# Kernel optimization log

Measured on AMD Instinct MI355X. Metric: run time of the kernel, lower is better.

The kernel has to match this reference:

```python
import jax, jax.numpy as jnp
import numpy as np

B, C, H, W = 4, 64, 256, 256
P, PRIOR, HID, HEADS, NPROMPT = 4, 64, 128, 4, 4
TOKEN = C * P * P  # 1024
RATIO = 0.25


def _patchify(x):
    b, c, h, w = x.shape
    gh, gw = h // P, w // P
    t = x.reshape(b, c, gh, P, gw, P).transpose(0, 2, 4, 1, 3, 5).reshape(b, gh * gw, c * P * P)
    return t, (b, c, gh, gw)


def _unpatchify(t, meta):
    b, c, gh, gw = meta
    return t.reshape(b, gh, gw, c, P, P).transpose(0, 3, 1, 4, 2, 5).reshape(b, c, gh * P, gw * P)


def _coords(gh, gw):
    ys = (jnp.arange(gh, dtype=jnp.float32) + 0.5) / gh
    xs = (jnp.arange(gw, dtype=jnp.float32) + 0.5) / gw
    yy, xx = jnp.meshgrid(ys, xs, indexing='ij')
    return jnp.stack([yy.ravel(), xx.ravel()], axis=-1)  # [N, 2]


def setup_inputs():
    key = jax.random.key(0)
    ks = iter(jax.random.split(key, 32))
    rn = lambda *s: jax.random.normal(next(ks), s, jnp.float32)
    w = lambda *s: rn(*s) * 0.02
    z = lambda *s: jnp.zeros(s, jnp.float32)
    return dict(
        vis_feat=rn(B, C, H, W),
        ir_feat=rn(B, C, H, W),
        prompt_bank=w(NPROMPT, PRIOR),
        Wr=w(2 * C, NPROMPT), br=z(NPROMPT),
        br_Wtok=w(2, 2 * TOKEN, HID), br_Wpri=w(2, PRIOR, HID), br_Wco=w(2, 2, HID),
        br_bs=z(2, HID), br_Wout=w(2, HID), br_bout=z(2),
        br_Wq=w(2, TOKEN, HID), br_Wk=w(2, TOKEN, HID), br_Wv=w(2, TOKEN, HID),
        br_Wo=w(2, HID, TOKEN), br_Wint=w(2, PRIOR, HID),
        br_Wbyp=w(2, 2 * TOKEN, TOKEN), br_bbyp=z(2, TOKEN),
        conv1_w=w(C, C, 3, 3), conv1_b=z(C),
        conv2_w=w(C, C, 3, 3), conv2_b=z(C),
        Wa1=w(PRIOR, 2 * C), ba1=z(2 * C),
        Wa2=w(2 * C, 2 * C), ba2=z(2 * C),
    )


def reference(vis_feat, ir_feat, prompt_bank, Wr, br, br_Wtok, br_Wpri, br_Wco, br_bs, br_Wout, br_bout, br_Wq, br_Wk, br_Wv, br_Wo, br_Wint, br_Wbyp, br_bbyp, conv1_w, conv1_b, conv2_w, conv2_b, Wa1, ba1, Wa2, ba2):
    # intent router: pooled features -> prompt mixture -> intent vector
    pooled = jnp.concatenate([vis_feat.mean((2, 3)), ir_feat.mean((2, 3))], -1)  # [B, 2C]
    prompt_weight = jax.nn.softmax(pooled @ Wr + br, -1)  # [B, NPROMPT]
    intent = prompt_weight @ prompt_bank  # [B, PRIOR]

    def split(x):
        F = jnp.fft.fft2(x)
        return jnp.abs(F), jnp.angle(F)

    vamp, vph = split(vis_feat)
    iamp, iph = split(ir_feat)

    def fuse(vm, im, i):
        vt, meta = _patchify(vm)
        it_, _ = _patchify(im)
        b, c, gh, gw = meta
        n = gh * gw
        coords = _coords(gh, gw)
        # token score net: tokens + intent + coord embedding -> scalar score per token
        h = (jnp.concatenate([vt, it_], -1) @ br_Wtok[i]
             + (intent @ br_Wpri[i])[:, None, :]
             + (coords @ br_Wco[i])[None] + br_bs[i])
        score = jax.nn.gelu(h) @ br_Wout[i] + br_bout[i]  # [B, N]
        k = max(1, int(n * RATIO))
        topk_val, topk_idx = jax.lax.top_k(score, k)
        gth = lambda t: jnp.take_along_axis(t, topk_idx[:, :, None], axis=1)
        vs, irs = gth(vt), gth(it_)  # [B, k, TOKEN]
        # selected-token cross attention (vis queries, ir keys/values), intent-modulated
        dh = HID // HEADS
        hd = lambda x, Wm: (x @ Wm).reshape(b, k, HEADS, dh)
        q, kk, vv = hd(vs, br_Wq[i]), hd(irs, br_Wk[i]), hd(irs, br_Wv[i])
        attn = jax.nn.softmax(jnp.einsum('bqhd,bkhd->bhqk', q, kk) / jnp.float32(np.sqrt(dh)), -1)
        o = jnp.einsum('bhqk,bkhd->bqhd', attn, vv).reshape(b, k, HID)
        o = o + (intent @ br_Wint[i])[:, None, :]
        fused_sel = vs + o @ br_Wo[i]  # [B, k, TOKEN]
        # lightweight bypass on all tokens (gated blend), then scatter selected back
        g = jax.nn.sigmoid(jnp.concatenate([vt, it_], -1) @ br_Wbyp[i] + br_bbyp[i])
        full = g * vt + (1.0 - g) * it_
        full = full.at[jnp.arange(b)[:, None], topk_idx].set(fused_sel)
        return _unpatchify(full, meta)

    famp = fuse(vamp, iamp, 0)
    fph = fuse(vph, iph, 1)
    fph = jnp.arctan2(jnp.sin(fph), jnp.cos(fph))  # phase wrap to (-pi, pi]
    spec = jax.lax.complex(famp * jnp.cos(fph), famp * jnp.sin(fph))
    spatial = jnp.fft.ifft2(spec).real

    conv = lambda x, wgt, bia: jax.lax.conv_general_dilated(
        x, wgt, (1, 1), 'SAME', dimension_numbers=('NCHW', 'OIHW', 'NCHW')) + bia[None, :, None, None]
    y = conv(jax.nn.relu(conv(spatial, conv1_w, conv1_b)), conv2_w, conv2_b)
    aff = jax.nn.gelu(intent @ Wa1 + ba1) @ Wa2 + ba2  # [B, 2C]
    gamma, beta = aff[:, :C], aff[:, C:]
    y = y * (1.0 + 0.1 * jnp.tanh(gamma))[:, :, None, None] + 0.1 * beta[:, :, None, None]
    return y + 0.5 * (vis_feat + ir_feat)
```

## Files before the change

kernel.cpp:

```cpp
#include <hip/hip_runtime.h>

typedef unsigned int uint;
typedef unsigned short ushort;
typedef unsigned long long u64;
typedef __attribute__((ext_vector_type(8))) short short8;
typedef __attribute__((ext_vector_type(4))) float f32x4;

__device__ __forceinline__ uint brev8(uint x){ return __brev(x) >> 24; }
__device__ __forceinline__ float geluf(float x){
  return 0.5f*x*(1.f + tanhf(0.7978845608028654f*(x + 0.044715f*x*x*x)));
}
__device__ __forceinline__ ushort f2bf(float f){
  unsigned u = __float_as_uint(f);
  unsigned r = u + 0x7FFFu + ((u >> 16) & 1u);
  return (ushort)(r >> 16);
}
__device__ __forceinline__ float bf2f(ushort u){
  return __uint_as_float((uint)u << 16);
}

__global__ __launch_bounds__(256) void kern_pool(const float* __restrict__ vis,
                                                 const float* __restrict__ irf,
                                                 float* __restrict__ pooled){
  __shared__ float red[256];
  int bc = blockIdx.x;
  int b = bc >> 7, cc = bc & 127;
  const float* src = (cc < 64) ? (vis + (size_t)(b*64+cc)*65536)
                               : (irf + (size_t)(b*64+(cc-64))*65536);
  float s = 0.f;
  for (int i = threadIdx.x; i < 65536; i += 256) s += src[i];
  red[threadIdx.x] = s;
  __syncthreads();
  for (int off = 128; off > 0; off >>= 1){
    if (threadIdx.x < off) red[threadIdx.x] += red[threadIdx.x + off];
    __syncthreads();
  }
  if (threadIdx.x == 0) pooled[bc] = red[0] * (1.f/65536.f);
}

__global__ __launch_bounds__(256) void kern_small(const float* __restrict__ pooled,
    const float* __restrict__ Wr, const float* __restrict__ br,
    const float* __restrict__ bank, const float* __restrict__ Wpri,
    const float* __restrict__ Wint, const float* __restrict__ Wa1,
    const float* __restrict__ ba1, const float* __restrict__ Wa2,
    const float* __restrict__ ba2,
    float* __restrict__ IP, float* __restrict__ IPint,
    float* __restrict__ modg, float* __restrict__ modb){
  __shared__ float logit_s[16];
  __shared__ float pw_s[16];
  __shared__ float intent_s[4][64];
  __shared__ float t1_s[4][128];
  int t = threadIdx.x;
  if (t < 16){
    int b = t >> 2, j = t & 3;
    float s = br[j];
    for (int k = 0; k < 128; ++k) s += pooled[b*128+k]*Wr[k*4+j];
    logit_s[t] = s;
  }
  __syncthreads();
  if (t < 4){
    int b = t;
    float m = logit_s[b*4];
    for (int j = 1; j < 4; ++j) m = fmaxf(m, logit_s[b*4+j]);
    float e[4], sum = 0.f;
    for (int j = 0; j < 4; ++j){ e[j] = expf(logit_s[b*4+j]-m); sum += e[j]; }
    for (int j = 0; j < 4; ++j) pw_s[b*4+j] = e[j]/sum;
  }
  __syncthreads();
  {
    int b = t >> 6, p = t & 63;
    float s = 0.f;
    for (int j = 0; j < 4; ++j) s += pw_s[b*4+j]*bank[j*64+p];
    intent_s[b][p] = s;
  }
  __syncthreads();
  for (int o = t; o < 1024; o += 256){
    int i = o >> 9, rem = o & 511, b = rem >> 7, n = rem & 127;
    float s1 = 0.f, s2 = 0.f;
    for (int p = 0; p < 64; ++p){
      float iv = intent_s[b][p];
      s1 += iv * Wpri[(i*64+p)*128 + n];
      s2 += iv * Wint[(i*64+p)*128 + n];
    }
    IP[o] = s1; IPint[o] = s2;
  }
  for (int o = t; o < 512; o += 256){
    int b = o >> 7, n = o & 127;
    float s = ba1[n];
    for (int p = 0; p < 64; ++p) s += intent_s[b][p]*Wa1[p*128+n];
    t1_s[b][n] = geluf(s);
  }
  __syncthreads();
  for (int o = t; o < 512; o += 256){
    int b = o >> 7, n = o & 127;
    float s = ba2[n];
    for (int p = 0; p < 128; ++p) s += t1_s[b][p]*Wa2[p*128+n];
    if (n < 64) modg[b*64+n] = 1.f + 0.1f*tanhf(s);
    else        modb[b*64+(n-64)] = 0.1f*s;
  }
}

__global__ __launch_bounds__(256) void kern_fft_rows_pack(const float* __restrict__ xv,
    const float* __restrict__ xi, float* __restrict__ sre, float* __restrict__ sim){
  __shared__ float re[2][256], im[2][256];
  __shared__ float twr[128], twi[128];
  int t = threadIdx.x;
  if (t < 128){
    float a = -6.2831853071795864f * (float)t * (1.f/256.f);
    sincosf(a, &twi[t], &twr[t]);
  }
  int r = t >> 7, jj = t & 127;
  size_t row = (size_t)blockIdx.x*2 + r;
  {
    const float* vp = xv + row*256;
    const float* ip = xi + row*256;
    re[r][jj] = vp[jj]; re[r][jj+128] = vp[jj+128];
    im[r][jj] = ip[jj]; im[r][jj+128] = ip[jj+128];
  }
  __syncthreads();
  for (int s = 0; s < 8; ++s){
    int half = 128 >> s;
    int j = jj & (half-1);
    int g = jj >> (7-s);
    int k = (g << (8-s)) + j;
    int m = j << s;
    float wc = twr[m], ws = twi[m];
    float are = re[r][k],      aim = im[r][k];
    float bre = re[r][k+half], bim = im[r][k+half];
    re[r][k] = are + bre; im[r][k] = aim + bim;
    float tr = are - bre, ti = aim - bim;
    re[r][k+half] = tr*wc - ti*ws;
    im[r][k+half] = tr*ws + ti*wc;
    __syncthreads();
  }
  {
    float* orp = sre + row*256; float* oip = sim + row*256;
    int w1 = jj, w2 = jj + 128;
    orp[w1] = re[r][brev8(w1)]; oip[w1] = im[r][brev8(w1)];
    orp[w2] = re[r][brev8(w2)]; oip[w2] = im[r][brev8(w2)];
  }
}

__global__ __launch_bounds__(256) void kern_fft_cols_pack(const float* __restrict__ sre,
    const float* __restrict__ sim, ushort* __restrict__ AV, ushort* __restrict__ PV,
    ushort* __restrict__ AI, ushort* __restrict__ PI){
  __shared__ float reL[256*17];
  __shared__ float imL[256*17];
  __shared__ float twr[128], twi[128];
  int t = threadIdx.x;
  if (t < 128){
    float a = -6.2831853071795864f * (float)t * (1.f/256.f);
    sincosf(a, &twi[t], &twr[t]);
  }
  int img = blockIdx.x >> 4;
  int j = blockIdx.x & 15;
  {
    const float* pr = sre + ((size_t)img*256 + t)*256;
    const float* pi = sim + ((size_t)img*256 + t)*256;
    int base = t*17;
    float4 a0 = *(const float4*)(pr + 8*j);
    float4 a1 = *(const float4*)(pr + 8*j + 4);
    float4 c0 = *(const float4*)(pi + 8*j);
    float4 c1 = *(const float4*)(pi + 8*j + 4);
    reL[base+0]=a0.x; reL[base+1]=a0.y; reL[base+2]=a0.z; reL[base+3]=a0.w;
    reL[base+4]=a1.x; reL[base+5]=a1.y; reL[base+6]=a1.z; reL[base+7]=a1.w;
    imL[base+0]=c0.x; imL[base+1]=c0.y; imL[base+2]=c0.z; imL[base+3]=c0.w;
    imL[base+4]=c1.x; imL[base+5]=c1.y; imL[base+6]=c1.z; imL[base+7]=c1.w;
    if (j == 0){
      reL[base+8] = pr[128]; imL[base+8] = pi[128];
      float4 b0 = *(const float4*)(pr + 248);
      float4 b1 = *(const float4*)(pr + 252);
      float4 d0 = *(const float4*)(pi + 248);
      float4 d1 = *(const float4*)(pi + 252);
      reL[base+9]=b0.y;  reL[base+10]=b0.z; reL[base+11]=b0.w;
      reL[base+12]=b1.x; reL[base+13]=b1.y; reL[base+14]=b1.z; reL[base+15]=b1.w;
      imL[base+9]=d0.y;  imL[base+10]=d0.z; imL[base+11]=d0.w;
      imL[base+12]=d1.x; imL[base+13]=d1.y; imL[base+14]=d1.z; imL[base+15]=d1.w;
    } else {
      float4 b0 = *(const float4*)(pr + 248 - 8*j);
      float4 b1 = *(const float4*)(pr + 252 - 8*j);
      float4 d0 = *(const float4*)(pi + 248 - 8*j);
      float4 d1 = *(const float4*)(pi + 252 - 8*j);
      reL[base+8]=b0.y;  reL[base+9]=b0.z;  reL[base+10]=b0.w;
      reL[base+11]=b1.x; reL[base+12]=b1.y; reL[base+13]=b1.z; reL[base+14]=b1.w;
      reL[base+15]=pr[256 - 8*j];
      imL[base+8]=d0.y;  imL[base+9]=d0.z;  imL[base+10]=d0.w;
      imL[base+11]=d1.x; imL[base+12]=d1.y; imL[base+13]=d1.z; imL[base+14]=d1.w;
      imL[base+15]=pi[256 - 8*j];
    }
  }
  __syncthreads();
  int col = t & 15, tb = t >> 4;
  for (int s = 0; s < 8; ++s){
    int half = 128 >> s;
    #pragma unroll
    for (int it = 0; it < 8; ++it){
      int tj = tb + it*16;
      int jl = tj & (half-1);
      int g = tj >> (7-s);
      int k = (g << (8-s)) + jl;
      int m = jl << s;
      float wc = twr[m], ws = twi[m];
      int i0 = k*17 + col, i1 = (k+half)*17 + col;
      float are = reL[i0], aim = imL[i0];
      float bre = reL[i1], bim = imL[i1];
      reL[i0] = are + bre; imL[i0] = aim + bim;
      float tr = are - bre, ti = aim - bim;
      reL[i1] = tr*wc - ti*ws;
      imL[i1] = tr*ws + ti*wc;
    }
    __syncthreads();
  }
  int b = img >> 6, cimg = img & 63;
  int u = t;
  int su  = (int)brev8((uint)u) * 17;
  int smu = (int)brev8((uint)((256 - u) & 255)) * 17;
  #pragma unroll
  for (int c = 0; c < 16; ++c){
    int v, mc;
    if (j == 0){
      v  = (c < 8) ? c : ((c == 8) ? 128 : 240 + c);
      mc = (c == 0) ? 0 : ((c == 8) ? 8 : 16 - c);
    } else {
      v  = (c < 8) ? (8*j + c) : (241 - 8*j + c);
      mc = 15 - c;
    }
    float re1 = reL[su + c],  im1 = imL[su + c];
    float re2 = reL[smu + mc], im2 = imL[smu + mc];
    float vr = 0.5f*(re1 + re2), vi = 0.5f*(im1 - im2);
    float jr = 0.5f*(im1 + im2), ji = 0.5f*(re2 - re1);
    float aV = sqrtf(vr*vr + vi*vi), pVh = atan2f(vi, vr);
    float aI = sqrtf(jr*jr + ji*ji), pIh = atan2f(ji, jr);
    size_t addr = ((size_t)(b*4096 + (u>>2)*64 + (v>>2)))*1024
                + cimg*16 + (u&3)*4 + (v&3);
    AV[addr] = f2bf(aV); PV[addr] = f2bf(pVh);
    AI[addr] = f2bf(aI); PI[addr] = f2bf(pIh);
  }
}

__global__ __launch_bounds__(256) void kern_ifft_rows_spec(const float* __restrict__ famp,
    const float* __restrict__ fph, float* __restrict__ sre, float* __restrict__ sim){
  __shared__ float re[4][256], im[4][256];
  __shared__ float twr[128], twi[128];
  int t = threadIdx.x;
  if (t < 128){
    float a = -6.2831853071795864f * (float)t * (1.f/256.f);
    sincosf(a, &twi[t], &twr[t]);
  }
  int R = blockIdx.x * 4;
  {
    int r = t >> 6, q = t & 63;
    int row = R + r;
    int bc = row >> 8, h = row & 255;
    int b = bc >> 6, c = bc & 63;
    size_t addr = ((size_t)(b*4096 + (h>>2)*64 + q))*1024 + c*16 + (h&3)*4;
    float4 a4 = *(const float4*)(famp + addr);
    float4 p4 = *(const float4*)(fph + addr);
    float sn, cs;
    sincosf(p4.x, &sn, &cs); re[r][4*q+0] = a4.x*cs; im[r][4*q+0] = a4.x*sn;
    sincosf(p4.y, &sn, &cs); re[r][4*q+1] = a4.y*cs; im[r][4*q+1] = a4.y*sn;
    sincosf(p4.z, &sn, &cs); re[r][4*q+2] = a4.z*cs; im[r][4*q+2] = a4.z*sn;
    sincosf(p4.w, &sn, &cs); re[r][4*q+3] = a4.w*cs; im[r][4*q+3] = a4.w*sn;
  }
  __syncthreads();
  for (int s = 0; s < 8; ++s){
    int half = 128 >> s;
    #pragma unroll
    for (int bi0 = 0; bi0 < 2; ++bi0){
      int bi = t + bi0*256;
      int r = bi >> 7, tj = bi & 127;
      int j = tj & (half-1);
      int g = tj >> (7-s);
      int k = (g << (8-s)) + j;
      int m = j << s;
      float wc = twr[m], ws = -twi[m];
      float are = re[r][k],      aim = im[r][k];
      float bre = re[r][k+half], bim = im[r][k+half];
      re[r][k] = are + bre; im[r][k] = aim + bim;
      float tr = are - bre, ti = aim - bim;
      re[r][k+half] = tr*wc - ti*ws;
      im[r][k+half] = tr*ws + ti*wc;
    }
    __syncthreads();
  }
  {
    int r = t >> 6, q = t & 63;
    size_t row = (size_t)R + r;
    float4 vr, vi;
    vr.x = re[r][brev8(4*q+0)]; vi.x = im[r][brev8(4*q+0)];
    vr.y = re[r][brev8(4*q+1)]; vi.y = im[r][brev8(4*q+1)];
    vr.z = re[r][brev8(4*q+2)]; vi.z = im[r][brev8(4*q+2)];
    vr.w = re[r][brev8(4*q+3)]; vi.w = im[r][brev8(4*q+3)];
    *(float4*)(sre + row*256 + 4*q) = vr;
    *(float4*)(sim + row*256 + 4*q) = vi;
  }
}

__global__ __launch_bounds__(256) void kern_fft_cols_inv(const float* __restrict__ sre,
    const float* __restrict__ sim, float* __restrict__ out0){
  __shared__ float reL[256*17];
  __shared__ float imL[256*17];
  __shared__ float twr[128], twi[128];
  int t = threadIdx.x;
  if (t < 128){
    float a = -6.2831853071795864f * (float)t * (1.f/256.f);
    sincosf(a, &twi[t], &twr[t]);
  }
  int img = blockIdx.x >> 4;
  int c0 = (blockIdx.x & 15) * 16;
  {
    const float* pr = sre + ((size_t)img*256 + t)*256 + c0;
    const float* pi = sim + ((size_t)img*256 + t)*256 + c0;
    #pragma unroll
    for (int p = 0; p < 4; ++p){
      float4 vr = *(const float4*)(pr + 4*p);
      float4 vi = *(const float4*)(pi + 4*p);
      int base = t*17 + 4*p;
      reL[base+0]=vr.x; reL[base+1]=vr.y; reL[base+2]=vr.z; reL[base+3]=vr.w;
      imL[base+0]=vi.x; imL[base+1]=vi.y; imL[base+2]=vi.z; imL[base+3]=vi.w;
    }
  }
  __syncthreads();
  int col = t & 15, tb = t >> 4;
  for (int s = 0; s < 8; ++s){
    int half = 128 >> s;
    #pragma unroll
    for (int it = 0; it < 8; ++it){
      int tj = tb + it*16;
      int j = tj & (half-1);
      int g = tj >> (7-s);
      int k = (g << (8-s)) + j;
      int m = j << s;
      float wc = twr[m];
      float ws = -twi[m];
      int i0 = k*17 + col, i1 = (k+half)*17 + col;
      float are = reL[i0], aim = imL[i0];
      float bre = reL[i1], bim = imL[i1];
      reL[i0] = are + bre; imL[i0] = aim + bim;
      float tr = are - bre, ti = aim - bim;
      reL[i1] = tr*wc - ti*ws;
      imL[i1] = tr*ws + ti*wc;
    }
    __syncthreads();
  }
  int h = t; int src = (int)brev8((uint)h);
  float* op = out0 + ((size_t)img*256 + h)*256 + c0;
  #pragma unroll
  for (int p = 0; p < 4; ++p){
    int base = src*17 + 4*p;
    float4 v;
    v.x = reL[base+0]*(1.f/65536.f);
    v.y = reL[base+1]*(1.f/65536.f);
    v.z = reL[base+2]*(1.f/65536.f);
    v.w = reL[base+3]*(1.f/65536.f);
    *(float4*)(op + 4*p) = v;
  }
}

struct TRS {
  const float* src[10];
  ushort* dst[10];
  int K[10], N[10];
  int start[11];
};
__global__ __launch_bounds__(256) void kern_tr(TRS p){
  __shared__ float lds[32][33];
  int bid = blockIdx.x;
  int e = 0;
  while (bid >= p.start[e+1]) ++e;
  int tloc = bid - p.start[e];
  int tilesN = p.N[e] >> 5;
  int tn = tloc % tilesN, tk = tloc / tilesN;
  int k0 = tk << 5, n0 = tn << 5;
  const float* src = p.src[e];
  ushort* dst = p.dst[e];
  int K = p.K[e], N = p.N[e];
  int r = threadIdx.x >> 5, c = threadIdx.x & 31;
  #pragma unroll
  for (int i = 0; i < 4; ++i)
    lds[r + 8*i][c] = src[(size_t)(k0 + r + 8*i)*N + n0 + c];
  __syncthreads();
  #pragma unroll
  for (int i = 0; i < 4; ++i)
    dst[(size_t)(n0 + r + 8*i)*K + k0 + c] = f2bf(lds[c][r + 8*i]);
}

struct GP2 {
  const ushort* A0[6];
  const ushort* Bt[6];
  float* Cm[6];
  const int* idxp[6];
  int N, K;
};

__global__ __launch_bounds__(256) void kern_mgemm2(GP2 p){
  __shared__ __align__(16) ushort Asb[64*64];
  __shared__ __align__(16) ushort Bsb[128*64];
  __shared__ int idx_s[64];
  int z = blockIdx.z;
  const ushort* A0 = p.A0[z];
  const ushort* Bt = p.Bt[z];
  float* Cm = p.Cm[z];
  int tid = threadIdx.x;
  int m0 = blockIdx.x * 64;
  int n0 = blockIdx.y * 128;
  int lane = tid & 63, w = tid >> 6;
  int wr = w & 1, wc = w >> 1;
  int lr = lane & 15, ql = lane >> 4;

  if (tid < 64){
    int m = m0 + tid;
    idx_s[tid] = p.idxp[z][(m >> 10)*1024 + (m & 1023)];
  }
  __syncthreads();
  int gb = m0 >> 10;

  f32x4 acc[2][4];
  #pragma unroll
  for (int i = 0; i < 2; ++i)
    #pragma unroll
    for (int j = 0; j < 4; ++j) acc[i][j] = (f32x4){0.f,0.f,0.f,0.f};

  int kh = tid & 7;
  int rA = tid >> 3;
  for (int k0 = 0; k0 < p.K; k0 += 64){
    #pragma unroll
    for (int s = 0; s < 2; ++s){
      int m = rA + 32*s;
      const ushort* ap = A0 + ((size_t)(gb << 12) + idx_s[m])*(size_t)p.K + k0 + kh*8;
      short8 v = *(const short8*)ap;
      int byte = m*128 + ((kh*16) ^ ((m & 7)*16));
      *(short8*)((char*)Asb + byte) = v;
    }
    #pragma unroll
    for (int s = 0; s < 4; ++s){
      int n = rA + 32*s;
      short8 v = *(const short8*)(Bt + (size_t)(n0+n)*p.K + k0 + kh*8);
      int byte = n*128 + ((kh*16) ^ ((n & 7)*16));
      *(short8*)((char*)Bsb + byte) = v;
    }
    __syncthreads();
    short8 af[2][2], bf[4][2];
    #pragma unroll
    for (int fm = 0; fm < 2; ++fm){
      int row = wr*32 + fm*16 + lr;
      #pragma unroll
      for (int kq = 0; kq < 2; ++kq){
        int byte = row*128 + ((kq*64 + ql*16) ^ ((row & 7)*16));
        af[fm][kq] = *(const short8*)((const char*)Asb + byte);
      }
    }
    #pragma unroll
    for (int fn = 0; fn < 4; ++fn){
      int row = wc*64 + fn*16 + lr;
      #pragma unroll
      for (int kq = 0; kq < 2; ++kq){
        int byte = row*128 + ((kq*64 + ql*16) ^ ((row & 7)*16));
        bf[fn][kq] = *(const short8*)((const char*)Bsb + byte);
      }
    }
    #pragma unroll
    for (int kq = 0; kq < 2; ++kq)
      #pragma unroll
      for (int fm = 0; fm < 2; ++fm)
        #pragma unroll
        for (int fn = 0; fn < 4; ++fn)
          acc[fm][fn] = __builtin_amdgcn_mfma_f32_16x16x32_bf16(af[fm][kq], bf[fn][kq],
                                                                acc[fm][fn], 0, 0, 0);
    __syncthreads();
  }

  #pragma unroll
  for (int fm = 0; fm < 2; ++fm){
    #pragma unroll
    for (int fn = 0; fn < 4; ++fn){
      int n = n0 + wc*64 + fn*16 + lr;
      #pragma unroll
      for (int reg = 0; reg < 4; ++reg){
        int m = m0 + wr*32 + fm*16 + ql*4 + reg;
        Cm[(size_t)m*p.N + n] = acc[fm][fn][reg];
      }
    }
  }
}

struct HSP {
  const ushort* A0[2];
  const ushort* A1[2];
  const ushort* Bt[2];
  float* score;
  const float* ep0[2];
  const float* ep1[2];
  const float* ep2[2];
  const float* wout;
  const float* bout;
  int Mper;
};

__global__ __launch_bounds__(256) void kern_hscore(HSP p){
  __shared__ __align__(16) ushort Asb[128*64];
  __shared__ __align__(16) ushort Bsb[128*64];
  __shared__ float part[2][128];
  int z = blockIdx.z;
  const ushort* Bt = p.Bt[z];
  int tid = threadIdx.x;
  int m0 = blockIdx.x * 128;
  int lane = tid & 63, w = tid >> 6;
  int wr = w & 1, wc = w >> 1;
  int lr = lane & 15, ql = lane >> 4;

  f32x4 acc[4][4];
  #pragma unroll
  for (int i = 0; i < 4; ++i)
    #pragma unroll
    for (int j = 0; j < 4; ++j) acc[i][j] = (f32x4){0.f,0.f,0.f,0.f};

  int kh = tid & 7;
  int rA = tid >> 3;
  for (int k0 = 0; k0 < 2048; k0 += 64){
    const ushort* Asrc = (k0 < 1024) ? p.A0[z] : p.A1[z];
    int kk = (k0 & 1023) + kh*8;
    #pragma unroll
    for (int s = 0; s < 4; ++s){
      int m = rA + 32*s;
      short8 v = *(const short8*)(Asrc + (size_t)(m0+m)*1024 + kk);
      int byte = m*128 + ((kh*16) ^ ((m & 7)*16));
      *(short8*)((char*)Asb + byte) = v;
    }
    #pragma unroll
    for (int s = 0; s < 4; ++s){
      int n = rA + 32*s;
      short8 v = *(const short8*)(Bt + (size_t)n*2048 + k0 + kh*8);
      int byte = n*128 + ((kh*16) ^ ((n & 7)*16));
      *(short8*)((char*)Bsb + byte) = v;
    }
    __syncthreads();
    short8 af[4][2], bf[4][2];
    #pragma unroll
    for (int fm = 0; fm < 4; ++fm){
      int row = wr*64 + fm*16 + lr;
      #pragma unroll
      for (int kq = 0; kq < 2; ++kq){
        int byte = row*128 + ((kq*64 + ql*16) ^ ((row & 7)*16));
        af[fm][kq] = *(const short8*)((const char*)Asb + byte);
      }
    }
    #pragma unroll
    for (int fn = 0; fn < 4; ++fn){
      int row = wc*64 + fn*16 + lr;
      #pragma unroll
      for (int kq = 0; kq < 2; ++kq){
        int byte = row*128 + ((kq*64 + ql*16) ^ ((row & 7)*16));
        bf[fn][kq] = *(const short8*)((const char*)Bsb + byte);
      }
    }
    #pragma unroll
    for (int kq = 0; kq < 2; ++kq)
      #pragma unroll
      for (int fm = 0; fm < 4; ++fm)
        #pragma unroll
        for (int fn = 0; fn < 4; ++fn)
          acc[fm][fn] = __builtin_amdgcn_mfma_f32_16x16x32_bf16(af[fm][kq], bf[fn][kq],
                                                                acc[fm][fn], 0, 0, 0);
    __syncthreads();
  }

  float wv[4];
  #pragma unroll
  for (int fn = 0; fn < 4; ++fn) wv[fn] = p.wout[z*128 + wc*64 + fn*16 + lr];
  #pragma unroll
  for (int fm = 0; fm < 4; ++fm){
    #pragma unroll
    for (int reg = 0; reg < 4; ++reg){
      int m = m0 + wr*64 + fm*16 + ql*4 + reg;
      int bl = m >> 12, g = m & 4095;
      int gy = g >> 6, gx = g & 63;
      float cy = ((float)gy + 0.5f)*(1.f/64.f);
      float cx = ((float)gx + 0.5f)*(1.f/64.f);
      float ps = 0.f;
      #pragma unroll
      for (int fn = 0; fn < 4; ++fn){
        int n = wc*64 + fn*16 + lr;
        float o = acc[fm][fn][reg] + p.ep0[z][bl*128 + n] + cy*p.ep1[z][n]
                + cx*p.ep1[z][128 + n] + p.ep2[z][n];
        ps += geluf(o)*wv[fn];
      }
      #pragma unroll
      for (int off = 8; off > 0; off >>= 1) ps += __shfl_xor(ps, off);
      if (lr == 0) part[wc][wr*64 + fm*16 + ql*4 + reg] = ps;
    }
  }
  __syncthreads();
  if (tid < 128)
    p.score[(size_t)z*p.Mper + m0 + tid] = part[0][tid] + part[1][tid] + p.bout[z];
}

struct BYP {
  const ushort* A0[2];
  const ushort* A1[2];
  const ushort* Bt[2];
  float* Cm[2];
  const int* nsel[2];
  const float* bias[2];
  const ushort* vt[2];
  const ushort* it[2];
};

__global__ __launch_bounds__(256) void kern_byp(BYP p){
  __shared__ __align__(16) ushort Asb[128*64];
  __shared__ __align__(16) ushort Bsb[128*64];
  __shared__ int idx_s[128];
  int z = blockIdx.z;
  const ushort* Bt = p.Bt[z];
  int tid = threadIdx.x;
  int gb  = blockIdx.x / 24;
  int m0l = (blockIdx.x % 24) * 128;
  int n0 = blockIdx.y * 128;
  int lane = tid & 63, w = tid >> 6;
  int wr = w & 1, wc = w >> 1;
  int lr = lane & 15, ql = lane >> 4;

  if (tid < 128)
    idx_s[tid] = p.nsel[z][(size_t)gb*3072 + m0l + tid];
  __syncthreads();

  f32x4 acc[4][4];
  #pragma unroll
  for (int i = 0; i < 4; ++i)
    #pragma unroll
    for (int j = 0; j < 4; ++j) acc[i][j] = (f32x4){0.f,0.f,0.f,0.f};

  int kh = tid & 7;
  int rA = tid >> 3;
  for (int k0 = 0; k0 < 2048; k0 += 64){
    const ushort* Asrc = (k0 < 1024) ? p.A0[z] : p.A1[z];
    int kk = (k0 & 1023) + kh*8;
    #pragma unroll
    for (int s = 0; s < 4; ++s){
      int m = rA + 32*s;
      size_t grow = (size_t)(gb << 12) + idx_s[m];
      short8 v = *(const short8*)(Asrc + grow*1024 + kk);
      int byte = m*128 + ((kh*16) ^ ((m & 7)*16));
      *(short8*)((char*)Asb + byte) = v;
    }
    #pragma unroll
    for (int s = 0; s < 4; ++s){
      int n = rA + 32*s;
      short8 v = *(const short8*)(Bt + (size_t)(n0+n)*2048 + k0 + kh*8);
      int byte = n*128 + ((kh*16) ^ ((n & 7)*16));
      *(short8*)((char*)Bsb + byte) = v;
    }
    __syncthreads();
    short8 af[4][2], bf[4][2];
    #pragma unroll
    for (int fm = 0; fm < 4; ++fm){
      int row = wr*64 + fm*16 + lr;
      #pragma unroll
      for (int kq = 0; kq < 2; ++kq){
        int byte = row*128 + ((kq*64 + ql*16) ^ ((row & 7)*16));
        af[fm][kq] = *(const short8*)((const char*)Asb + byte);
      }
    }
    #pragma unroll
    for (int fn = 0; fn < 4; ++fn){
      int row = wc*64 + fn*16 + lr;
      #pragma unroll
      for (int kq = 0; kq < 2; ++kq){
        int byte = row*128 + ((kq*64 + ql*16) ^ ((row & 7)*16));
        bf[fn][kq] = *(const short8*)((const char*)Bsb + byte);
      }
    }
    #pragma unroll
    for (int kq = 0; kq < 2; ++kq)
      #pragma unroll
      for (int fm = 0; fm < 4; ++fm)
        #pragma unroll
        for (int fn = 0; fn < 4; ++fn)
          acc[fm][fn] = __builtin_amdgcn_mfma_f32_16x16x32_bf16(af[fm][kq], bf[fn][kq],
                                                                acc[fm][fn], 0, 0, 0);
    __syncthreads();
  }

  float* Cm = p.Cm[z];
  const ushort* vtp = p.vt[z];
  const ushort* itp = p.it[z];
  #pragma unroll
  for (int fm = 0; fm < 4; ++fm){
    #pragma unroll
    for (int fn = 0; fn < 4; ++fn){
      int n = n0 + wc*64 + fn*16 + lr;
      float bia = p.bias[z][n];
      #pragma unroll
      for (int reg = 0; reg < 4; ++reg){
        int mloc = wr*64 + fm*16 + ql*4 + reg;
        size_t off = ((size_t)(gb << 12) + idx_s[mloc])*1024 + n;
        float vt = bf2f(vtp[off]);
        float it = bf2f(itp[off]);
        float gg = 1.f/(1.f + expf(-(acc[fm][fn][reg] + bia)));
        Cm[off] = gg*vt + (1.f-gg)*it;
      }
    }
  }
}

struct SCP {
  const float* A0[2];
  const float* Bm[2];
  float* Cm[2];
  const int* idxp[2];
  const ushort* vtb[2];
};

__global__ __launch_bounds__(256) void kern_scat(SCP p){
  __shared__ __align__(16) ushort Asb[64*40];
  __shared__ __align__(16) ushort Bsb[128*40];
  __shared__ int idx_s[64];
  int z = blockIdx.z;
  const float* A0 = p.A0[z];
  const float* Bm = p.Bm[z];
  float* Cm = p.Cm[z];
  int tid = threadIdx.x;
  int m0 = blockIdx.y * 64;
  int n0 = blockIdx.x * 128;
  int lane = tid & 63, w = tid >> 6;
  int wr = w & 1, wc = w >> 1;
  int lr = lane & 15, ql = lane >> 4;
  if (tid < 64){
    int m = m0 + tid;
    idx_s[tid] = p.idxp[z][(m >> 10)*1024 + (m & 1023)];
  }
  __syncthreads();
  int gb = m0 >> 10;

  f32x4 acc[2][4];
  #pragma unroll
  for (int i = 0; i < 2; ++i)
    #pragma unroll
    for (int j = 0; j < 4; ++j) acc[i][j] = (f32x4){0.f,0.f,0.f,0.f};

  for (int k0 = 0; k0 < 128; k0 += 32){
    {
      int m = tid & 63;
      int khh = (tid >> 6) * 8;
      const float* ap = A0 + (size_t)(m0+m)*128 + k0 + khh;
      float4 f0 = *(const float4*)ap;
      float4 f1 = *(const float4*)(ap + 4);
      short8 v;
      v[0]=(short)f2bf(f0.x); v[1]=(short)f2bf(f0.y);
      v[2]=(short)f2bf(f0.z); v[3]=(short)f2bf(f0.w);
      v[4]=(short)f2bf(f1.x); v[5]=(short)f2bf(f1.y);
      v[6]=(short)f2bf(f1.z); v[7]=(short)f2bf(f1.w);
      *(short8*)&Asb[m*40 + khh] = v;
    }
    #pragma unroll
    for (int e0 = 0; e0 < 512; e0 += 256){
      int e = e0 + tid;
      int n = e & 127;
      int khh = (e >> 7) * 8;
      const float* bp = Bm + (size_t)(k0+khh)*1024 + n0 + n;
      short8 v;
      #pragma unroll
      for (int j = 0; j < 8; ++j) v[j] = (short)f2bf(bp[(size_t)j*1024]);
      *(short8*)&Bsb[n*40 + khh] = v;
    }
    __syncthreads();
    short8 af[2], bf[4];
    #pragma unroll
    for (int fr = 0; fr < 2; ++fr)
      af[fr] = *(const short8*)&Asb[(wr*32 + fr*16 + lr)*40 + ql*8];
    #pragma unroll
    for (int fc = 0; fc < 4; ++fc)
      bf[fc] = *(const short8*)&Bsb[(wc*64 + fc*16 + lr)*40 + ql*8];
    #pragma unroll
    for (int fr = 0; fr < 2; ++fr)
      #pragma unroll
      for (int fc = 0; fc < 4; ++fc)
        acc[fr][fc] = __builtin_amdgcn_mfma_f32_16x16x32_bf16(af[fr], bf[fc],
                                                              acc[fr][fc], 0, 0, 0);
    __syncthreads();
  }

  #pragma unroll
  for (int fr = 0; fr < 2; ++fr){
    #pragma unroll
    for (int fc = 0; fc < 4; ++fc){
      int n = n0 + wc*64 + fc*16 + lr;
      #pragma unroll
      for (int reg = 0; reg < 4; ++reg){
        int mloc = wr*32 + fr*16 + ql*4 + reg;
        int gt = idx_s[mloc];
        size_t off = ((size_t)(gb << 12) + gt)*1024 + n;
        Cm[off] = acc[fr][fc][reg] + bf2f(p.vtb[z][off]);
      }
    }
  }
}

__global__ __launch_bounds__(1024) void kern_topk(const float* __restrict__ score,
    int* __restrict__ idx_out, int* __restrict__ nsel_out){
  __shared__ u64 keys[4096];
  int b = blockIdx.x, t = threadIdx.x;
  for (int i = t; i < 4096; i += 1024){
    float s = score[b*4096 + i];
    uint u = __float_as_uint(s);
    uint msk = (u & 0x80000000u) ? ~u : (u | 0x80000000u);
    keys[i] = ((u64)msk << 32) | (uint)(4095 - i);
  }
  __syncthreads();
  for (int k = 2; k <= 4096; k <<= 1){
    for (int j = k >> 1; j > 0; j >>= 1){
      for (int i = t; i < 4096; i += 1024){
        int l = i ^ j;
        if (l > i){
          u64 a = keys[i], c = keys[l];
          bool descB = ((i & k) == 0);
          bool sw = descB ? (a < c) : (a > c);
          if (sw){ keys[i] = c; keys[l] = a; }
        }
      }
      __syncthreads();
    }
  }
  idx_out[b*1024 + t] = 4095 - (int)(keys[t] & 0xFFFFFFFFu);
  for (int i = t; i < 3072; i += 1024)
    nsel_out[(size_t)b*3072 + i] = 4095 - (int)(keys[1024 + i] & 0xFFFFFFFFu);
}

__global__ __launch_bounds__(128) void kern_attn_part(const float* __restrict__ qb,
    const float* __restrict__ kb, const float* __restrict__ vb,
    float* __restrict__ paoa, float* __restrict__ pml){
  __shared__ float Ks[64][32];
  __shared__ float Vs[64][32];
  int t = threadIdx.x;
  int hh = blockIdx.y;
  int zc = blockIdx.z;
  int zf = zc >> 2, c = zc & 3;
  size_t boff = (size_t)zf*131072;
  int jq = blockIdx.x*128 + t;
  float qv[32];
  {
    const float4* qp = (const float4*)(qb + boff + (size_t)jq*128 + hh*32);
    #pragma unroll
    for (int d = 0; d < 8; ++d) ((float4*)qv)[d] = qp[d];
  }
  float mrun = -3.0e38f, lrun = 0.f;
  float oa[32];
  #pragma unroll
  for (int d = 0; d < 32; ++d) oa[d] = 0.f;
  for (int kt = 0; kt < 4; ++kt){
    int k0 = c*256 + kt*64;
    #pragma unroll
    for (int rep = 0; rep < 4; ++rep){
      int f = t + rep*128;
      int r = f >> 3, q4 = f & 7;
      size_t base = boff + (size_t)(k0 + r)*128 + hh*32 + 4*q4;
      *(float4*)&Ks[r][4*q4] = *(const float4*)(kb + base);
      *(float4*)&Vs[r][4*q4] = *(const float4*)(vb + base);
    }
    __syncthreads();
    #pragma unroll
    for (int st = 0; st < 4; ++st){
      float s[16];
      #pragma unroll
      for (int j = 0; j < 16; ++j){
        float v = 0.f;
        #pragma unroll
        for (int d = 0; d < 32; ++d) v += qv[d]*Ks[st*16+j][d];
        s[j] = v * 0.17677669529663687f;
      }
      float mt = s[0];
      #pragma unroll
      for (int j = 1; j < 16; ++j) mt = fmaxf(mt, s[j]);
      float mnew = fmaxf(mrun, mt);
      float alpha = expf(mrun - mnew);
      lrun *= alpha;
      #pragma unroll
      for (int d = 0; d < 32; ++d) oa[d] *= alpha;
      #pragma unroll
      for (int j = 0; j < 16; ++j){
        float pe = expf(s[j] - mnew);
        lrun += pe;
        #pragma unroll
        for (int d = 0; d < 32; ++d) oa[d] += pe*Vs[st*16+j][d];
      }
      mrun = mnew;
    }
    __syncthreads();
  }
  size_t rec = (((size_t)zf*4 + hh)*4 + c)*1024 + jq;
  float* pp = paoa + rec*32;
  #pragma unroll
  for (int d = 0; d < 8; ++d) ((float4*)pp)[d] = ((float4*)oa)[d];
  pml[rec*2]   = mrun;
  pml[rec*2+1] = lrun;
}

__global__ __launch_bounds__(256) void kern_attn_comb(const float* __restrict__ paoa,
    const float* __restrict__ pml, float* __restrict__ ob,
    const float* __restrict__ ipint, int PB, int b0){
  int t = threadIdx.x;
  int hh = blockIdx.y, zf = blockIdx.z;
  int jq = blockIdx.x*256 + t;
  size_t rbase = (((size_t)zf*4 + hh)*4)*1024 + jq;
  float mc[4], lc[4];
  #pragma unroll
  for (int c = 0; c < 4; ++c){
    mc[c] = pml[(rbase + c*1024)*2];
    lc[c] = pml[(rbase + c*1024)*2 + 1];
  }
  float M = fmaxf(fmaxf(mc[0], mc[1]), fmaxf(mc[2], mc[3]));
  float wgt[4], L = 0.f;
  #pragma unroll
  for (int c = 0; c < 4; ++c){ wgt[c] = expf(mc[c] - M); L += lc[c]*wgt[c]; }
  float inv = 1.f/L;
  int br = (zf >= PB) ? 1 : 0;
  int bb = zf - br*PB;
  const float* ip = ipint + br*512 + (b0+bb)*128 + hh*32;
  float* op = ob + (size_t)zf*131072 + (size_t)jq*128 + hh*32;
  #pragma unroll
  for (int d = 0; d < 32; ++d){
    float o = 0.f;
    #pragma unroll
    for (int c = 0; c < 4; ++c) o += paoa[(rbase + c*1024)*32 + d]*wgt[c];
    op[d] = o*inv + ip[d];
  }
}

__global__ __launch_bounds__(256) void kern_wt(const float* __restrict__ w1,
    const float* __restrict__ w2, ushort* __restrict__ wt){
  int blk = blockIdx.x;
  const float* src = (blk < 9) ? w1 : w2;
  int tap = blk - (blk < 9 ? 0 : 9);
  ushort* dst = wt + (blk < 9 ? 0 : 36864) + tap*4096;
  for (int e = threadIdx.x; e < 4096; e += 256){
    dst[e] = f2bf(src[(size_t)e*9 + tap]);
  }
}

template<int MODE>
__global__ __launch_bounds__(256) void kern_cmfma(const float* __restrict__ in,
    const ushort* __restrict__ wt, const float* __restrict__ bias,
    float* __restrict__ out,
    const float* __restrict__ modg, const float* __restrict__ modb,
    const float* __restrict__ vis, const float* __restrict__ irf){
  __shared__ __align__(16) ushort ins[64][268];
  int t = threadIdx.x;
  int y = blockIdx.x, b = blockIdx.y;
  int lane = t & 63, w = t >> 6;
  int wc = w & 1, wx = w >> 1;
  int lr = lane & 15, ql = lane >> 4;

  f32x4 acc[2][8];
  #pragma unroll
  for (int f = 0; f < 2; ++f)
    #pragma unroll
    for (int xf = 0; xf < 8; ++xf) acc[f][xf] = (f32x4){0.f,0.f,0.f,0.f};

  for (int dy = 0; dy < 3; ++dy){
    int yy = y + dy - 1;
    if (yy < 0 || yy > 255) continue;
    const float* src = in + ((size_t)(b*64)*256 + yy)*256;
    #pragma unroll
    for (int s = 0; s < 16; ++s){
      int e = t + s*256;
      int ci = e >> 6, q = e & 63;
      float4 f4 = *(const float4*)(src + (size_t)ci*65536 + 4*q);
      uint lo = (uint)f2bf(f4.x) | ((uint)f2bf(f4.y) << 16);
      uint hi = (uint)f2bf(f4.z) | ((uint)f2bf(f4.w) << 16);
      *(uint2*)&ins[ci][4*q + 4] = make_uint2(lo, hi);
    }
    if (t < 128){
      int r = t & 63;
      ins[r][(t >> 6) ? 260 : 3] = 0;
    }
    __syncthreads();
    short8 wf[2][3][2];
    #pragma unroll
    for (int kk = 0; kk < 2; ++kk)
      #pragma unroll
      for (int dx = 0; dx < 3; ++dx)
        #pragma unroll
        for (int f = 0; f < 2; ++f)
          wf[kk][dx][f] = *(const short8*)(wt +
            (size_t)((dy*3 + dx)*64 + 32*wc + 16*f + lr)*64 + kk*32 + ql*8);
    #pragma unroll
    for (int kk = 0; kk < 2; ++kk){
      const ushort* bp = &ins[kk*32 + ql*8][0];
      #pragma unroll
      for (int dx = 0; dx < 3; ++dx){
        int xb = 128*wx + lr + dx + 3;
        #pragma unroll
        for (int xf = 0; xf < 8; ++xf){
          int xi = xb + 16*xf;
          short8 bf;
          #pragma unroll
          for (int e = 0; e < 8; ++e) bf[e] = (short)bp[e*268 + xi];
          acc[0][xf] = __builtin_amdgcn_mfma_f32_16x16x32_bf16(wf[kk][dx][0], bf,
                                                               acc[0][xf], 0, 0, 0);
          acc[1][xf] = __builtin_amdgcn_mfma_f32_16x16x32_bf16(wf[kk][dx][1], bf,
                                                               acc[1][xf], 0, 0, 0);
        }
      }
    }
    __syncthreads();
  }

  #pragma unroll
  for (int f = 0; f < 2; ++f){
    #pragma unroll
    for (int xf = 0; xf < 8; ++xf){
      int x = 128*wx + 16*xf + lr;
      #pragma unroll
      for (int reg = 0; reg < 4; ++reg){
        int co = 32*wc + 16*f + ql*4 + reg;
        float v = acc[f][xf][reg] + bias[co];
        size_t oi = ((size_t)(b*64 + co)*256 + y)*256 + x;
        if (MODE == 1){
          out[oi] = fmaxf(v, 0.f);
        } else {
          out[oi] = v*modg[b*64+co] + modb[b*64+co] + 0.5f*(vis[oi] + irf[oi]);
        }
      }
    }
  }
}

extern "C" void kernel_launch(void* const* d_in, const int* in_sizes, int n_in,
                              void* d_out, int out_size, void* d_ws, size_t ws_size,
                              hipStream_t stream){
  (void)in_sizes; (void)n_in; (void)out_size;
  const float* vis  = (const float*)d_in[0];
  const float* irf  = (const float*)d_in[1];
  const float* bank = (const float*)d_in[2];
  const float* Wr   = (const float*)d_in[3];
  const float* br   = (const float*)d_in[4];
  const float* Wtok = (const float*)d_in[5];
  const float* Wpri = (const float*)d_in[6];
  const float* Wco  = (const float*)d_in[7];
  const float* bs   = (const float*)d_in[8];
  const float* Wout = (const float*)d_in[9];
  const float* bout = (const float*)d_in[10];
  const float* Wq   = (const float*)d_in[11];
  const float* Wk   = (const float*)d_in[12];
  const float* Wv   = (const float*)d_in[13];
  const float* Wo   = (const float*)d_in[14];
  const float* Wint = (const float*)d_in[15];
  const float* Wbyp = (const float*)d_in[16];
  const float* bbyp = (const float*)d_in[17];
  const float* c1w  = (const float*)d_in[18];
  const float* c1b  = (const float*)d_in[19];
  const float* c2w  = (const float*)d_in[20];
  const float* c2b  = (const float*)d_in[21];
  const float* Wa1  = (const float*)d_in[22];
  const float* ba1  = (const float*)d_in[23];
  const float* Wa2  = (const float*)d_in[24];
  const float* ba2  = (const float*)d_in[25];

  auto needB = [](int PB)->size_t{
    return ((size_t)PB*14755840 + 2792448) * 4;
  };
  const int PB = (ws_size >= needB(4)) ? 4 : (ws_size >= needB(2)) ? 2 : 1;

  float* ws = (float*)d_ws;
  const size_t PLF = (size_t)PB*4194304;
  float* PH4 = ws;
  ushort* ABV = (ushort*)(ws + PLF);
  ushort* PBV = ABV + PLF;
  ushort* ABI = PBV + PLF;
  ushort* PBI = ABI + PLF;
  float* S0 = ws + PLF;
  float* S1 = S0 + PLF;
  float* sm = ws + 3*PLF;
  float* hbuf  = sm; sm += (size_t)2*PB*524288;
  float* qbuf  = sm; sm += (size_t)2*PB*131072;
  float* kbuf  = sm; sm += (size_t)2*PB*131072;
  float* vbuf  = sm; sm += (size_t)2*PB*131072;
  float* obuf  = sm; sm += (size_t)2*PB*131072;
  float* score = sm; sm += (size_t)2*PB*4096;
  int*   idxb  = (int*)sm; sm += (size_t)2*PB*1024;
  float* pml   = sm; sm += (size_t)PB*65536;
  ushort* BTtok = (ushort*)sm;
  ushort* BTbyp = BTtok + 524288;
  ushort* BTq   = BTbyp + 4194304;
  ushort* BTk   = BTq + 262144;
  ushort* BTv   = BTk + 262144;
  sm += 2752512;
  float* pooled= sm; sm += 512;
  float* IP    = sm; sm += 1024;
  float* IPint = sm; sm += 1024;
  float* modg  = sm; sm += 256;
  float* modb  = sm; sm += 256;
  ushort* wtb = (ushort*)sm; sm += 36864;
  int*   nselb = (int*)hbuf;
  float* paoa  = hbuf;

  kern_pool <<<512, 256, 0, stream>>>(vis, irf, pooled);
  kern_small<<<1, 256, 0, stream>>>(pooled, Wr, br, bank, Wpri, Wint,
                                    Wa1, ba1, Wa2, ba2, IP, IPint, modg, modb);
  kern_wt   <<<18, 256, 0, stream>>>(c1w, c2w, wtb);
  {
    TRS tr{};
    const float* srcs[10] = {Wtok, Wtok+262144, Wbyp, Wbyp+2097152,
                             Wq, Wq+131072, Wk, Wk+131072, Wv, Wv+131072};
    ushort* dsts[10] = {BTtok, BTtok+262144, BTbyp, BTbyp+2097152,
                        BTq, BTq+131072, BTk, BTk+131072, BTv, BTv+131072};
    int Ks[10] = {2048,2048,2048,2048,1024,1024,1024,1024,1024,1024};
    int Ns[10] = {128,128,1024,1024,128,128,128,128,128,128};
    int tiles[10] = {256,256,2048,2048,128,128,128,128,128,128};
    int acc0 = 0;
    for (int i = 0; i < 10; ++i){
      tr.src[i] = srcs[i]; tr.dst[i] = dsts[i];
      tr.K[i] = Ks[i]; tr.N[i] = Ns[i];
      tr.start[i] = acc0; acc0 += tiles[i];
    }
    tr.start[10] = acc0;
    kern_tr<<<acc0, 256, 0, stream>>>(tr);
  }

  for (int b0 = 0; b0 < 4; b0 += PB){
    const float* vis_b = vis + (size_t)b0*4194304;
    const float* ir_b  = irf + (size_t)b0*4194304;
    float* OUT = (float*)d_out + (size_t)b0*4194304;

    kern_fft_rows_pack<<<PB*8192, 256, 0, stream>>>(vis_b, ir_b, OUT, PH4);
    kern_fft_cols_pack<<<PB*1024, 256, 0, stream>>>(OUT, PH4, ABV, PBV, ABI, PBI);

    {
      HSP p{};
      p.A0[0]=ABV; p.A1[0]=ABI; p.A0[1]=PBV; p.A1[1]=PBI;
      for (int z = 0; z < 2; ++z){
        p.Bt[z] = BTtok + (size_t)z*262144;
        p.ep0[z] = IP + z*512 + b0*128;
        p.ep1[z] = Wco + z*256;
        p.ep2[z] = bs + z*128;
      }
      p.score = score; p.wout = Wout; p.bout = bout;
      p.Mper = PB*4096;
      kern_hscore<<<dim3(PB*32, 1, 2), 256, 0, stream>>>(p);
    }
    kern_topk<<<2*PB, 1024, 0, stream>>>(score, idxb, nselb);
    {
      BYP p{};
      p.A0[0]=ABV; p.A1[0]=ABI; p.A0[1]=PBV; p.A1[1]=PBI;
      p.vt[0]=ABV; p.it[0]=ABI; p.vt[1]=PBV; p.it[1]=PBI;
      p.Cm[0]=OUT; p.Cm[1]=PH4;
      for (int z = 0; z < 2; ++z){
        p.Bt[z] = BTbyp + (size_t)z*2097152;
        p.bias[z] = bbyp + z*1024;
        p.nsel[z] = nselb + (size_t)z*PB*3072;
      }
      kern_byp<<<dim3(PB*24, 8, 2), 256, 0, stream>>>(p);
    }
    {
      GP2 p{};
      const ushort* Aplanes[6] = {ABV, ABI, ABI, PBV, PBI, PBI};
      const ushort* Bmats[6] = {BTq, BTk, BTv, BTq+131072, BTk+131072, BTv+131072};
      float* Cms[6] = {qbuf, kbuf, vbuf,
                       qbuf+(size_t)PB*131072, kbuf+(size_t)PB*131072,
                       vbuf+(size_t)PB*131072};
      for (int z = 0; z < 6; ++z){
        p.A0[z] = Aplanes[z]; p.Bt[z] = Bmats[z]; p.Cm[z] = Cms[z];
        p.idxp[z] = idxb + (z < 3 ? 0 : PB*1024);
      }
      p.N = 128; p.K = 1024;
      kern_mgemm2<<<dim3(PB*16, 1, 6), 256, 0, stream>>>(p);
    }
    kern_attn_part<<<dim3(8, 4, 2*PB*4), 128, 0, stream>>>(qbuf, kbuf, vbuf,
                                                           paoa, pml);
    kern_attn_comb<<<dim3(4, 4, 2*PB), 256, 0, stream>>>(paoa, pml, obuf,
                                                         IPint, PB, b0);
    {
      SCP p{};
      p.A0[0]=obuf; p.A0[1]=obuf+(size_t)PB*131072;
      p.Bm[0]=Wo; p.Bm[1]=Wo+131072;
      p.Cm[0]=OUT; p.Cm[1]=PH4;
      p.vtb[0]=ABV; p.vtb[1]=PBV;
      p.idxp[0]=idxb; p.idxp[1]=idxb+PB*1024;
      kern_scat<<<dim3(8, PB*16, 2), 256, 0, stream>>>(p);
    }

    kern_ifft_rows_spec<<<PB*4096, 256, 0, stream>>>(OUT, PH4, S0, S1);
    kern_fft_cols_inv  <<<PB*1024, 256, 0, stream>>>(S0, S1, OUT);
  }

  kern_cmfma<1><<<dim3(256, 4), 256, 0, stream>>>((float*)d_out, wtb, c1b, ws,
                                                  nullptr, nullptr, nullptr, nullptr);
  kern_cmfma<2><<<dim3(256, 4), 256, 0, stream>>>(ws, wtb + 36864, c2b, (float*)d_out,
                                                  modg, modb, vis, irf);
}
```

Measured before the change: 1.291 ms.

## Restructure column-FFT pack: uniform column sets, swizzled LDS, vectorized bf16 stores

Reworks the column FFT and pack kernel so every block loads a uniform set of 18 columns (two 8-wide runs plus two mirror columns) instead of special-casing j==0. Rows in LDS use a stride of 19 with an XOR swizzle to cut bank conflicts. Butterfly work is spread as 9 iterations over idx%18 / idx/18, which adds integer divides and some redundant column work. The output stage packs four bf16 values into one 8-byte store per tensor, so each block does one wide write where it previously did four scalar 2-byte writes.

```diff
diff --git a/kernel.cpp b/kernel.cpp
--- a/kernel.cpp
+++ b/kernel.cpp
@@ -144,8 +144,8 @@
 __global__ __launch_bounds__(256) void kern_fft_cols_pack(const float* __restrict__ sre,
     const float* __restrict__ sim, ushort* __restrict__ AV, ushort* __restrict__ PV,
     ushort* __restrict__ AI, ushort* __restrict__ PI){
-  __shared__ float reL[256*17];
-  __shared__ float imL[256*17];
+  __shared__ float reL[256*19];
+  __shared__ float imL[256*19];
   __shared__ float twr[128], twi[128];
   int t = threadIdx.x;
   if (t < 128){
@@ -154,87 +154,97 @@
   }
   int img = blockIdx.x >> 4;
   int j = blockIdx.x & 15;
+  int vA = 8*j;
+  int vB = 248 - 8*j;
+  int v16 = (256 - 8*j) & 255;
+  int v17 = 8*j + 8;
   {
     const float* pr = sre + ((size_t)img*256 + t)*256;
     const float* pi = sim + ((size_t)img*256 + t)*256;
-    int base = t*17;
-    float4 a0 = *(const float4*)(pr + 8*j);
-    float4 a1 = *(const float4*)(pr + 8*j + 4);
-    float4 c0 = *(const float4*)(pi + 8*j);
-    float4 c1 = *(const float4*)(pi + 8*j + 4);
+    int base = (t ^ (t >> 4))*19;
+    float4 a0 = *(const float4*)(pr + vA);
+    float4 a1 = *(const float4*)(pr + vA + 4);
+    float4 c0 = *(const float4*)(pi + vA);
+    float4 c1 = *(const float4*)(pi + vA + 4);
     reL[base+0]=a0.x; reL[base+1]=a0.y; reL[base+2]=a0.z; reL[base+3]=a0.w;
     reL[base+4]=a1.x; reL[base+5]=a1.y; reL[base+6]=a1.z; reL[base+7]=a1.w;
     imL[base+0]=c0.x; imL[base+1]=c0.y; imL[base+2]=c0.z; imL[base+3]=c0.w;
     imL[base+4]=c1.x; imL[base+5]=c1.y; imL[base+6]=c1.z; imL[base+7]=c1.w;
-    if (j == 0){
-      reL[base+8] = pr[128]; imL[base+8] = pi[128];
-      float4 b0 = *(const float4*)(pr + 248);
-      float4 b1 = *(const float4*)(pr + 252);
-      float4 d0 = *(const float4*)(pi + 248);
-      float4 d1 = *(const float4*)(pi + 252);
-      reL[base+9]=b0.y;  reL[base+10]=b0.z; reL[base+11]=b0.w;
-      reL[base+12]=b1.x; reL[base+13]=b1.y; reL[base+14]=b1.z; reL[base+15]=b1.w;
-      imL[base+9]=d0.y;  imL[base+10]=d0.z; imL[base+11]=d0.w;
-      imL[base+12]=d1.x; imL[base+13]=d1.y; imL[base+14]=d1.z; imL[base+15]=d1.w;
-    } else {
-      float4 b0 = *(const float4*)(pr + 248 - 8*j);
-      float4 b1 = *(const float4*)(pr + 252 - 8*j);
-      float4 d0 = *(const float4*)(pi + 248 - 8*j);
-      float4 d1 = *(const float4*)(pi + 252 - 8*j);
-      reL[base+8]=b0.y;  reL[base+9]=b0.z;  reL[base+10]=b0.w;
-      reL[base+11]=b1.x; reL[base+12]=b1.y; reL[base+13]=b1.z; reL[base+14]=b1.w;
-      reL[base+15]=pr[256 - 8*j];
-      imL[base+8]=d0.y;  imL[base+9]=d0.z;  imL[base+10]=d0.w;
-      imL[base+11]=d1.x; imL[base+12]=d1.y; imL[base+13]=d1.z; imL[base+14]=d1.w;
-      imL[base+15]=pi[256 - 8*j];
-    }
-  }
-  __syncthreads();
-  int col = t & 15, tb = t >> 4;
+    float4 b0 = *(const float4*)(pr + vB);
+    float4 b1 = *(const float4*)(pr + vB + 4);
+    float4 d0 = *(const float4*)(pi + vB);
+    float4 d1 = *(const float4*)(pi + vB + 4);
+    reL[base+8]=b0.x;  reL[base+9]=b0.y;  reL[base+10]=b0.z; reL[base+11]=b0.w;
+    reL[base+12]=b1.x; reL[base+13]=b1.y; reL[base+14]=b1.z; reL[base+15]=b1.w;
+    imL[base+8]=d0.x;  imL[base+9]=d0.y;  imL[base+10]=d0.z; imL[base+11]=d0.w;
+    imL[base+12]=d1.x; imL[base+13]=d1.y; imL[base+14]=d1.z; imL[base+15]=d1.w;
+    reL[base+16] = pr[v16]; imL[base+16] = pi[v16];
+    reL[base+17] = pr[v17]; imL[base+17] = pi[v17];
+  }
+  __syncthreads();
   for (int s = 0; s < 8; ++s){
     int half = 128 >> s;
     #pragma unroll
-    for (int it = 0; it < 8; ++it){
-      int tj = tb + it*16;
+    for (int it = 0; it < 9; ++it){
+      int idx = t + it*256;
+      int col = idx % 18;
+      int tj  = idx / 18;
       int jl = tj & (half-1);
-      int g = tj >> (7-s);
-      int k = (g << (8-s)) + jl;
-      int m = jl << s;
+      int g  = tj >> (7-s);
+      int k  = (g << (8-s)) + jl;
+      int m  = jl << s;
       float wc = twr[m], ws = twi[m];
-      int i0 = k*17 + col, i1 = (k+half)*17 + col;
-      float are = reL[i0], aim = imL[i0];
-      float bre = reL[i1], bim = imL[i1];
-      reL[i0] = are + bre; imL[i0] = aim + bim;
+      int r1 = k + half;
+      int p0 = (k  ^ (k  >> 4))*19 + col;
+      int p1 = (r1 ^ (r1 >> 4))*19 + col;
+      float are = reL[p0], aim = imL[p0];
+      float bre = reL[p1], bim = imL[p1];
+      reL[p0] = are + bre; imL[p0] = aim + bim;
       float tr = are - bre, ti = aim - bim;
-      reL[i1] = tr*wc - ti*ws;
-      imL[i1] = tr*ws + ti*wc;
+      reL[p1] = tr*wc - ti*ws;
+      imL[p1] = tr*ws + ti*wc;
     }
     __syncthreads();
   }
   int b = img >> 6, cimg = img & 63;
   int u = t;
-  int su  = (int)brev8((uint)u) * 17;
-  int smu = (int)brev8((uint)((256 - u) & 255)) * 17;
-  #pragma unroll
-  for (int c = 0; c < 16; ++c){
-    int v, mc;
-    if (j == 0){
-      v  = (c < 8) ? c : ((c == 8) ? 128 : 240 + c);
-      mc = (c == 0) ? 0 : ((c == 8) ? 8 : 16 - c);
-    } else {
-      v  = (c < 8) ? (8*j + c) : (241 - 8*j + c);
-      mc = 15 - c;
-    }
-    float re1 = reL[su + c],  im1 = imL[su + c];
-    float re2 = reL[smu + mc], im2 = imL[smu + mc];
-    float vr = 0.5f*(re1 + re2), vi = 0.5f*(im1 - im2);
-    float jr = 0.5f*(im1 + im2), ji = 0.5f*(re2 - re1);
-    float aV = sqrtf(vr*vr + vi*vi), pVh = atan2f(vi, vr);
-    float aI = sqrtf(jr*jr + ji*ji), pIh = atan2f(ji, jr);
-    size_t addr = ((size_t)(b*4096 + (u>>2)*64 + (v>>2)))*1024
-                + cimg*16 + (u&3)*4 + (v&3);
-    AV[addr] = f2bf(aV); PV[addr] = f2bf(pVh);
-    AI[addr] = f2bf(aI); PI[addr] = f2bf(pIh);
+  int bu  = (int)brev8((uint)u);
+  int bmu = (int)brev8((uint)((256 - u) & 255));
+  int su  = (bu  ^ (bu  >> 4))*19;
+  int smu = (bmu ^ (bmu >> 4))*19;
+  #pragma unroll
+  for (int qi = 0; qi < 4; ++qi){
+    int cbase = qi*4;
+    int vbase = (qi < 2) ? (vA + qi*4) : (vB + (qi-2)*4);
+    ushort av4[4], pv4[4], ai4[4], pi4[4];
+    #pragma unroll
+    for (int e = 0; e < 4; ++e){
+      int c = cbase + e;
+      int mc = (c == 0) ? 16 : ((c == 8) ? 17 : (16 - c));
+      float re1 = reL[su + c],   im1 = imL[su + c];
+      float re2 = reL[smu + mc], im2 = imL[smu + mc];
+      float vr = 0.5f*(re1 + re2), vi = 0.5f*(im1 - im2);
+      float jr = 0.5f*(im1 + im2), ji = 0.5f*(re2 - re1);
+      av4[e] = f2bf(sqrtf(vr*vr + vi*vi));
+      pv4[e] = f2bf(atan2f(vi, vr));
+      ai4[e] = f2bf(sqrtf(jr*jr + ji*ji));
+      pi4[e] = f2bf(atan2f(ji, jr));
+    }
+    size_t addr = ((size_t)(b*4096 + (u>>2)*64 + (vbase>>2)))*1024
+                + cimg*16 + (u&3)*4;
+    uint2 w;
+    w.x = (uint)av4[0] | ((uint)av4[1]<<16);
+    w.y = (uint)av4[2] | ((uint)av4[3]<<16);
+    *(uint2*)(AV + addr) = w;
+    w.x = (uint)pv4[0] | ((uint)pv4[1]<<16);
+    w.y = (uint)pv4[2] | ((uint)pv4[3]<<16);
+    *(uint2*)(PV + addr) = w;
+    w.x = (uint)ai4[0] | ((uint)ai4[1]<<16);
+    w.y = (uint)ai4[2] | ((uint)ai4[3]<<16);
+    *(uint2*)(AI + addr) = w;
+    w.x = (uint)pi4[0] | ((uint)pi4[1]<<16);
+    w.y = (uint)pi4[2] | ((uint)pi4[3]<<16);
+    *(uint2*)(PI + addr) = w;
   }
 }
 
```

New measurement: 1.231 ms. 4.7% less time.
